# Optimization experiments

Measured on AMD Instinct MI355X. Metric: run time of the kernel, lower is better.

The kernel has to match this reference:

```python
import jax, jax.numpy as jnp
import numpy as np

B, S, D = 1, 2048, 4096
NH, NKV, HD = 32, 8, 128
N_REP = NH // NKV
NEG = -1e9


def setup_inputs() -> dict:
    key = jax.random.key(0)
    ks = jax.random.split(key, 8)
    x = jax.random.normal(ks[0], (B, S, D), dtype=jnp.float32)
    # rotary freqs (theta=10000), shape [S, HD//2]
    inv = 1.0 / (10000.0 ** (jnp.arange(0, HD, 2, dtype=jnp.float32) / HD))
    ang = jnp.arange(S, dtype=jnp.float32)[:, None] * inv[None, :]
    freqs_cos, freqs_sin = jnp.cos(ang), jnp.sin(ang)
    # causal mask [1,1,S,S]
    row = jnp.arange(S)[:, None]
    col = jnp.arange(S)[None, :]
    mask = jnp.where(col <= row, 0.0, NEG).astype(jnp.float32)[None, None]
    input_indexes = jnp.arange(S, dtype=jnp.int64)
    cache_k = jnp.zeros((B, S, NKV, HD), dtype=jnp.float32)
    cache_v = jnp.zeros((B, S, NKV, HD), dtype=jnp.float32)
    sc = 0.02
    wq = jax.random.normal(ks[1], (NH * HD, D), dtype=jnp.float32) * sc
    wk = jax.random.normal(ks[2], (NKV * HD, D), dtype=jnp.float32) * sc
    wv = jax.random.normal(ks[3], (NKV * HD, D), dtype=jnp.float32) * sc
    wo = jax.random.normal(ks[4], (NH * HD, D), dtype=jnp.float32).T * sc
    return {"x": x, "freqs_cos": freqs_cos, "freqs_sin": freqs_sin, "mask": mask,
            "input_indexes": input_indexes, "cache_k": cache_k, "cache_v": cache_v,
            "wq": wq, "wk": wk, "wv": wv, "wo": wo}


def _rope(t, cos, sin):
    # t: [B,S,H,HD]; treat last dim as HD//2 complex pairs (even=real, odd=imag)
    tr = t.reshape(*t.shape[:-1], HD // 2, 2)
    xr, xi = tr[..., 0], tr[..., 1]
    c = cos[None, :, None, :]  # [1,S,1,HD//2]
    s = sin[None, :, None, :]
    outr = xr * c - xi * s
    outi = xr * s + xi * c
    return jnp.stack([outr, outi], axis=-1).reshape(t.shape)


def reference(x, freqs_cos, freqs_sin, mask, input_indexes, cache_k, cache_v, wq, wk, wv, wo):
    bsz, seqlen = x.shape[0], x.shape[-2]
    xq = (x @ wq.T).reshape(bsz, seqlen, NH, HD)
    xk = (x @ wk.T).reshape(bsz, seqlen, NKV, HD)
    xv = (x @ wv.T).reshape(bsz, seqlen, NKV, HD)
    xq = _rope(xq, freqs_cos, freqs_sin)
    xk = _rope(xk, freqs_cos, freqs_sin)
    # KV-cache append (index_copy along seq dim)
    cache_k = cache_k.at[:, input_indexes].set(xk)
    cache_v = cache_v.at[:, input_indexes].set(xv)
    # GQA: repeat kv heads
    keys = jnp.repeat(cache_k, N_REP, axis=2)    # [B,S,NH,HD]
    values = jnp.repeat(cache_v, N_REP, axis=2)
    scores = jnp.einsum('bshd,bthd->bhst', xq, keys) / jnp.sqrt(jnp.float32(HD))
    scores = scores + mask
    probs = jax.nn.softmax(scores.astype(jnp.float32), axis=-1).astype(xq.dtype)
    out = jnp.einsum('bhst,bthd->bhsd', probs, values)
    out = out.transpose(0, 2, 1, 3).reshape(bsz, seqlen, -1)
    return (out @ wo.T, cache_k, cache_v)
```

## Files before the change

### kernel.cpp

```cpp
#include <hip/hip_runtime.h>
#include <cstdint>

#define S_LEN 2048
#define D_DIM 4096
#define NH_ 32
#define NKV_ 8
#define HD_ 128
#define GK 4096

typedef unsigned short u16;
typedef __attribute__((ext_vector_type(4))) float f32x4;
typedef __attribute__((ext_vector_type(8))) short bf16x8;
typedef __attribute__((ext_vector_type(4))) short s16x4;

__device__ __forceinline__ short f2bf(float f) {
  union { float f; unsigned int u; } v; v.f = f;
  unsigned int r = v.u + 0x7fffu + ((v.u >> 16) & 1u);
  return (short)(r >> 16);
}

__device__ __forceinline__ void glds16(const void* g, void* l) {
  __builtin_amdgcn_global_load_lds(
      (const __attribute__((address_space(1))) void*)g,
      (__attribute__((address_space(3))) void*)l, 16, 0, 0);
}

__global__ __launch_bounds__(256) void cvt_bf16(const float* __restrict__ src,
                                                u16* __restrict__ dst, int n8) {
  int i = blockIdx.x * 256 + threadIdx.x;
  if (i < n8) {
    float4 a = *(const float4*)&src[(size_t)i * 8];
    float4 b = *(const float4*)&src[(size_t)i * 8 + 4];
    bf16x8 o = { f2bf(a.x), f2bf(a.y), f2bf(a.z), f2bf(a.w),
                 f2bf(b.x), f2bf(b.y), f2bf(b.z), f2bf(b.w) };
    *(bf16x8*)&dst[(size_t)i * 8] = o;
  }
}

template <int MODE>
__global__ __launch_bounds__(256) void gemm_bf(const u16* __restrict__ A,
                                               const u16* __restrict__ W,
                                               float* __restrict__ C,
                                               u16* __restrict__ qbf,
                                               u16* __restrict__ kbf,
                                               u16* __restrict__ vbf,
                                               float* __restrict__ cko,
                                               float* __restrict__ cvo,
                                               const float* __restrict__ fc,
                                               const float* __restrict__ fs,
                                               int N) {
  __shared__ __align__(16) u16 As[128 * 64];
  __shared__ __align__(16) u16 Bs[128 * 64];
  const int t = threadIdx.x;
  const int lane = t & 63;
  const int wave = t >> 6;
  const int wm = (wave >> 1) * 64;
  const int wn = (wave & 1) * 64;
  const int quad = lane >> 4;
  const int L = lane & 15;
  const int bm = blockIdx.y * 128;
  const int bn = blockIdx.x * 128;
  const int dr = lane >> 3;
  const int cb = lane & 7;
  const int cbs = cb ^ dr;

  f32x4 acc[4][4];
#pragma unroll
  for (int i = 0; i < 4; ++i)
#pragma unroll
    for (int j = 0; j < 4; ++j) { f32x4 z = {0.f, 0.f, 0.f, 0.f}; acc[i][j] = z; }

  for (int k0 = 0; k0 < GK; k0 += 64) {
    __syncthreads();
#pragma unroll
    for (int q = 0; q < 4; ++q) {
      int chunk = wave * 4 + q;
      int row = chunk * 8 + dr;
      glds16(&A[(size_t)(bm + row) * GK + k0 + cbs * 8], &As[chunk * 512]);
      glds16(&W[(size_t)(bn + row) * GK + k0 + cbs * 8], &Bs[chunk * 512]);
    }
    __syncthreads();
#pragma unroll
    for (int s = 0; s < 2; ++s) {
      bf16x8 af[4], bw[4];
#pragma unroll
      for (int i = 0; i < 4; ++i)
        af[i] = *(const bf16x8*)&As[(wm + 16 * i + L) * 64 + (((s * 4 + quad) ^ (L & 7)) * 8)];
#pragma unroll
      for (int j = 0; j < 4; ++j)
        bw[j] = *(const bf16x8*)&Bs[(wn + 16 * j + L) * 64 + (((s * 4 + quad) ^ (L & 7)) * 8)];
#pragma unroll
      for (int i = 0; i < 4; ++i)
#pragma unroll
        for (int j = 0; j < 4; ++j)
          acc[i][j] = __builtin_amdgcn_mfma_f32_16x16x32_bf16(af[i], bw[j], acc[i][j], 0, 0, 0);
    }
  }

  if (MODE == 0) {
#pragma unroll
    for (int i = 0; i < 4; ++i) {
      int r0 = bm + wm + i * 16 + quad * 4;
#pragma unroll
      for (int j = 0; j < 4; ++j) {
        int c = bn + wn + j * 16 + L;
#pragma unroll
        for (int r = 0; r < 4; ++r) C[(size_t)(r0 + r) * N + c] = acc[i][j][r];
      }
    }
  } else {
    const float scale = 0.08838834764831845f;
#pragma unroll
    for (int i = 0; i < 4; ++i) {
#pragma unroll
      for (int j = 0; j < 4; ++j) {
        int c = bn + wn + 16 * j + L;
#pragma unroll
        for (int r = 0; r < 4; ++r) {
          int srow = bm + wm + 16 * i + 4 * quad + r;
          float v = acc[i][j][r];
          float partner = __shfl_xor(v, 1);
          if (c < 4096) {
            int p = (c >> 1) & 63;
            float co = fc[srow * 64 + p], si = fs[srow * 64 + p];
            float out = (c & 1) ? partner * si + v * co : v * co - partner * si;
            qbf[(size_t)srow * 4096 + c] = (u16)f2bf(out * scale);
          } else if (c < 5120) {
            int p = (c >> 1) & 63;
            float co = fc[srow * 64 + p], si = fs[srow * 64 + p];
            float out = (c & 1) ? partner * si + v * co : v * co - partner * si;
            int cc = c - 4096;
            cko[(size_t)srow * 1024 + cc] = out;
            kbf[(size_t)srow * 1024 + cc] = (u16)f2bf(out);
          } else {
            int cc = c - 5120;
            cvo[(size_t)srow * 1024 + cc] = v;
            vbf[(size_t)srow * 1024 + cc] = (u16)f2bf(v);
          }
        }
      }
    }
  }
}

__global__ __launch_bounds__(256, 3) void attn_bf(const u16* __restrict__ qbf,
                                                  const u16* __restrict__ kbf,
                                                  const u16* __restrict__ vbf,
                                                  u16* __restrict__ ao) {
  __shared__ __align__(16) u16 Ks[64 * 136];
  __shared__ __align__(16) u16 Vt[128 * 64];
  __shared__ __align__(16) u16 Ps[4 * 16 * 72];
  const int t = threadIdx.x;
  const int wave = t >> 6;
  const int lane = t & 63;
  const int Q4 = lane >> 4;
  const int L = lane & 15;
  const int h = blockIdx.y;
  const int qb = 31 - (int)blockIdx.x;
  const int kvh = h >> 2;
  const int qs0 = qb * 64;
  u16* Psw = &Ps[wave * 16 * 72];

  bf16x8 qf[4];
  {
    const u16* qbase = &qbf[(size_t)(qs0 + 16 * wave + L) * D_DIM + h * HD_ + 8 * Q4];
#pragma unroll
    for (int s = 0; s < 4; ++s) qf[s] = *(const bf16x8*)&qbase[32 * s];
  }

  f32x4 o[8];
#pragma unroll
  for (int jd = 0; jd < 8; ++jd) { f32x4 z = {0.f, 0.f, 0.f, 0.f}; o[jd] = z; }
  float mold[4] = {-1e30f, -1e30f, -1e30f, -1e30f};
  float lst[4] = {0.f, 0.f, 0.f, 0.f};

  for (int kt = 0; kt <= qb; ++kt) {
    __syncthreads();
    const u16* kb = &kbf[(size_t)(kt * 64) * (NKV_ * HD_) + kvh * HD_];
    const u16* vb = &vbf[(size_t)(kt * 64) * (NKV_ * HD_) + kvh * HD_];
#pragma unroll
    for (int p = 0; p < 4; ++p) {
      int u = t + 256 * p;
      int r = u >> 4, c8 = u & 15;
      *(bf16x8*)&Ks[r * 136 + c8 * 8] =
          *(const bf16x8*)&kb[(size_t)r * (NKV_ * HD_) + c8 * 8];
    }
#pragma unroll
    for (int p = 0; p < 4; ++p) {
      int u = t + 256 * p;
      int d = u & 127, bb = u >> 7;
      const u16* vsrc = &vb[(size_t)(bb * 8) * (NKV_ * HD_) + d];
      short vv[8];
#pragma unroll
      for (int j = 0; j < 8; ++j) vv[j] = (short)vsrc[(size_t)j * (NKV_ * HD_)];
      bf16x8 pk = { vv[0], vv[1], vv[2], vv[3], vv[4], vv[5], vv[6], vv[7] };
      *(bf16x8*)&Vt[d * 64 + ((bb + d) & 7) * 8] = pk;
    }
    __syncthreads();

    f32x4 sa[4];
#pragma unroll
    for (int jn = 0; jn < 4; ++jn) { f32x4 z = {0.f, 0.f, 0.f, 0.f}; sa[jn] = z; }
#pragma unroll
    for (int s = 0; s < 4; ++s) {
#pragma unroll
      for (int jn = 0; jn < 4; ++jn) {
        bf16x8 kf = *(const bf16x8*)&Ks[(16 * jn + L) * 136 + 32 * s + 8 * Q4];
        sa[jn] = __builtin_amdgcn_mfma_f32_16x16x32_bf16(qf[s], kf, sa[jn], 0, 0, 0);
      }
    }

    const int gq0 = qs0 + 16 * wave + 4 * Q4;
    const int gk0 = kt * 64 + L;
    float rmax[4];
#pragma unroll
    for (int r = 0; r < 4; ++r) {
#pragma unroll
      for (int jn = 0; jn < 4; ++jn)
        if (gk0 + 16 * jn > gq0 + r) sa[jn][r] = -1e30f;
      rmax[r] = fmaxf(fmaxf(sa[0][r], sa[1][r]), fmaxf(sa[2][r], sa[3][r]));
    }
#pragma unroll
    for (int m = 1; m < 16; m <<= 1) {
#pragma unroll
      for (int r = 0; r < 4; ++r) rmax[r] = fmaxf(rmax[r], __shfl_xor(rmax[r], m));
    }
    float p_[4][4], rsum[4], alpha[4];
#pragma unroll
    for (int r = 0; r < 4; ++r) {
      float mnew = fmaxf(mold[r], rmax[r]);
      alpha[r] = __expf(mold[r] - mnew);
#pragma unroll
      for (int jn = 0; jn < 4; ++jn) p_[jn][r] = __expf(sa[jn][r] - mnew);
      rsum[r] = (p_[0][r] + p_[1][r]) + (p_[2][r] + p_[3][r]);
      mold[r] = mnew;
    }
#pragma unroll
    for (int m = 1; m < 16; m <<= 1) {
#pragma unroll
      for (int r = 0; r < 4; ++r) rsum[r] += __shfl_xor(rsum[r], m);
    }
#pragma unroll
    for (int r = 0; r < 4; ++r) lst[r] = lst[r] * alpha[r] + rsum[r];
#pragma unroll
    for (int jd = 0; jd < 8; ++jd)
#pragma unroll
      for (int r = 0; r < 4; ++r) o[jd][r] *= alpha[r];

#pragma unroll
    for (int r = 0; r < 4; ++r)
#pragma unroll
      for (int jn = 0; jn < 4; ++jn)
        Psw[(4 * Q4 + r) * 72 + 16 * jn + L] = (u16)f2bf(p_[jn][r]);
    asm volatile("s_waitcnt lgkmcnt(0)" ::: "memory");

#pragma unroll
    for (int s2 = 0; s2 < 2; ++s2) {
      bf16x8 pa = *(const bf16x8*)&Psw[L * 72 + 32 * s2 + 8 * Q4];
#pragma unroll
      for (int jd = 0; jd < 8; ++jd) {
        bf16x8 vf = *(const bf16x8*)&Vt[(16 * jd + L) * 64 + ((4 * s2 + Q4 + L) & 7) * 8];
        o[jd] = __builtin_amdgcn_mfma_f32_16x16x32_bf16(pa, vf, o[jd], 0, 0, 0);
      }
    }
  }

  float inv[4];
#pragma unroll
  for (int r = 0; r < 4; ++r) inv[r] = 1.0f / lst[r];
#pragma unroll
  for (int r = 0; r < 4; ++r) {
    u16* dst = &ao[(size_t)(qs0 + 16 * wave + 4 * Q4 + r) * D_DIM + h * HD_ + L];
#pragma unroll
    for (int jd = 0; jd < 8; ++jd) dst[16 * jd] = (u16)f2bf(o[jd][r] * inv[r]);
  }
}

#define LDA 40
__global__ __launch_bounds__(256) void gemm_bt(const float* __restrict__ A,
                                               const float* __restrict__ W,
                                               float* __restrict__ C, int N) {
  __shared__ short As[128 * LDA];
  __shared__ short Bs[128 * LDA];
  const int t = threadIdx.x;
  const int lane = t & 63;
  const int wave = t >> 6;
  const int wm = (wave >> 1) * 64;
  const int wn = (wave & 1) * 64;
  const int quad = lane >> 4;
  const int l15 = lane & 15;
  const int bm = blockIdx.y * 128;
  const int bn = blockIdx.x * 128;
  f32x4 acc[4][4];
#pragma unroll
  for (int i = 0; i < 4; ++i)
#pragma unroll
    for (int j = 0; j < 4; ++j) { f32x4 z = {0.f, 0.f, 0.f, 0.f}; acc[i][j] = z; }
  for (int k0 = 0; k0 < GK; k0 += 32) {
    __syncthreads();
#pragma unroll
    for (int p = 0; p < 4; ++p) {
      int idx = p * 256 + t;
      int row = idx >> 3;
      int c4 = (idx & 7) * 4;
      const float4 av = *(const float4*)&A[(size_t)(bm + row) * GK + k0 + c4];
      const float4 wv = *(const float4*)&W[(size_t)(bn + row) * GK + k0 + c4];
      s16x4 a4 = { f2bf(av.x), f2bf(av.y), f2bf(av.z), f2bf(av.w) };
      s16x4 w4 = { f2bf(wv.x), f2bf(wv.y), f2bf(wv.z), f2bf(wv.w) };
      *(s16x4*)&As[row * LDA + c4] = a4;
      *(s16x4*)&Bs[row * LDA + c4] = w4;
    }
    __syncthreads();
    bf16x8 af[4], bfr[4];
#pragma unroll
    for (int i = 0; i < 4; ++i) {
      af[i]  = *(const bf16x8*)&As[(wm + i * 16 + l15) * LDA + quad * 8];
      bfr[i] = *(const bf16x8*)&Bs[(wn + i * 16 + l15) * LDA + quad * 8];
    }
#pragma unroll
    for (int i = 0; i < 4; ++i)
#pragma unroll
      for (int j = 0; j < 4; ++j)
        acc[i][j] = __builtin_amdgcn_mfma_f32_16x16x32_bf16(af[i], bfr[j], acc[i][j], 0, 0, 0);
  }
#pragma unroll
  for (int i = 0; i < 4; ++i) {
    int r0 = bm + wm + i * 16 + quad * 4;
#pragma unroll
    for (int j = 0; j < 4; ++j) {
      int c = bn + wn + j * 16 + l15;
#pragma unroll
      for (int r = 0; r < 4; ++r) C[(size_t)(r0 + r) * N + c] = acc[i][j][r];
    }
  }
}

__global__ __launch_bounds__(256) void rope_kernel(float* __restrict__ xq,
                                                   const float* __restrict__ xk,
                                                   float* __restrict__ cko,
                                                   const float* __restrict__ fc,
                                                   const float* __restrict__ fs) {
  int i = blockIdx.x * 256 + threadIdx.x;
  const int NQP = S_LEN * NH_ * (HD_ / 2);
  if (i < NQP) {
    int s = i >> 11; int rem = i & 2047; int p = rem & 63;
    float c = fc[s * 64 + p], sn = fs[s * 64 + p];
    float2 v = *(const float2*)&xq[(size_t)s * D_DIM + 2 * rem];
    *(float2*)&xq[(size_t)s * D_DIM + 2 * rem] =
        make_float2(v.x * c - v.y * sn, v.x * sn + v.y * c);
  } else {
    int j = i - NQP; int s = j >> 9; int rem = j & 511; int p = rem & 63;
    float c = fc[s * 64 + p], sn = fs[s * 64 + p];
    float2 v = *(const float2*)&xk[(size_t)s * (NKV_ * HD_) + 2 * rem];
    *(float2*)&cko[(size_t)s * (NKV_ * HD_) + 2 * rem] =
        make_float2(v.x * c - v.y * sn, v.x * sn + v.y * c);
  }
}

__global__ __launch_bounds__(256, 3) void attn_mfma(const float* __restrict__ xq,
                                                    const float* __restrict__ ck,
                                                    const float* __restrict__ cv,
                                                    float* __restrict__ outp) {
  __shared__ __align__(16) short Ks[64 * 136];
  __shared__ __align__(16) short Vt[128 * 64];
  __shared__ __align__(16) short Ps[4 * 16 * 72];
  const int t = threadIdx.x;
  const int wave = t >> 6;
  const int lane = t & 63;
  const int Q4 = lane >> 4;
  const int L = lane & 15;
  const int h = blockIdx.y;
  const int qb = 31 - (int)blockIdx.x;
  const int kvh = h >> 2;
  const int qs0 = qb * 64;
  const float scale = 0.08838834764831845f;
  short* Psw = &Ps[wave * 16 * 72];
  bf16x8 qf[4];
  {
    const float* qbase = &xq[(size_t)(qs0 + 16 * wave + L) * D_DIM + h * HD_ + 8 * Q4];
#pragma unroll
    for (int s = 0; s < 4; ++s) {
      float4 a = *(const float4*)&qbase[32 * s];
      float4 b = *(const float4*)&qbase[32 * s + 4];
      bf16x8 q8 = { f2bf(a.x * scale), f2bf(a.y * scale), f2bf(a.z * scale), f2bf(a.w * scale),
                    f2bf(b.x * scale), f2bf(b.y * scale), f2bf(b.z * scale), f2bf(b.w * scale) };
      qf[s] = q8;
    }
  }
  f32x4 o[8];
#pragma unroll
  for (int jd = 0; jd < 8; ++jd) { f32x4 z = {0.f, 0.f, 0.f, 0.f}; o[jd] = z; }
  float mold[4] = {-1e30f, -1e30f, -1e30f, -1e30f};
  float lst[4] = {0.f, 0.f, 0.f, 0.f};
  for (int kt = 0; kt <= qb; ++kt) {
    __syncthreads();
    const float* ckb = &ck[(size_t)(kt * 64) * (NKV_ * HD_) + kvh * HD_];
    const float* cvb = &cv[(size_t)(kt * 64) * (NKV_ * HD_) + kvh * HD_];
#pragma unroll
    for (int p = 0; p < 8; ++p) {
      int i = t + 256 * p;
      int r = i >> 5, c4 = (i & 31) * 4;
      float4 v = *(const float4*)&ckb[(size_t)r * (NKV_ * HD_) + c4];
      s16x4 k4 = { f2bf(v.x), f2bf(v.y), f2bf(v.z), f2bf(v.w) };
      *(s16x4*)&Ks[r * 136 + c4] = k4;
    }
#pragma unroll
    for (int p = 0; p < 4; ++p) {
      int u = t + 256 * p;
      int d = u & 127, bb = u >> 7;
      float vv[8];
#pragma unroll
      for (int j = 0; j < 8; ++j) vv[j] = cvb[(size_t)(bb * 8 + j) * (NKV_ * HD_) + d];
      bf16x8 pk = { f2bf(vv[0]), f2bf(vv[1]), f2bf(vv[2]), f2bf(vv[3]),
                    f2bf(vv[4]), f2bf(vv[5]), f2bf(vv[6]), f2bf(vv[7]) };
      *(bf16x8*)&Vt[d * 64 + ((bb + d) & 7) * 8] = pk;
    }
    __syncthreads();
    f32x4 sa[4];
#pragma unroll
    for (int jn = 0; jn < 4; ++jn) { f32x4 z = {0.f, 0.f, 0.f, 0.f}; sa[jn] = z; }
#pragma unroll
    for (int s = 0; s < 4; ++s) {
#pragma unroll
      for (int jn = 0; jn < 4; ++jn) {
        bf16x8 kf = *(const bf16x8*)&Ks[(16 * jn + L) * 136 + 32 * s + 8 * Q4];
        sa[jn] = __builtin_amdgcn_mfma_f32_16x16x32_bf16(qf[s], kf, sa[jn], 0, 0, 0);
      }
    }
    const int gq0 = qs0 + 16 * wave + 4 * Q4;
    const int gk0 = kt * 64 + L;
    float rmax[4];
#pragma unroll
    for (int r = 0; r < 4; ++r) {
#pragma unroll
      for (int jn = 0; jn < 4; ++jn)
        if (gk0 + 16 * jn > gq0 + r) sa[jn][r] = -1e30f;
      rmax[r] = fmaxf(fmaxf(sa[0][r], sa[1][r]), fmaxf(sa[2][r], sa[3][r]));
    }
#pragma unroll
    for (int m = 1; m < 16; m <<= 1) {
#pragma unroll
      for (int r = 0; r < 4; ++r) rmax[r] = fmaxf(rmax[r], __shfl_xor(rmax[r], m));
    }
    float p_[4][4], rsum[4], alpha[4];
#pragma unroll
    for (int r = 0; r < 4; ++r) {
      float mnew = fmaxf(mold[r], rmax[r]);
      alpha[r] = __expf(mold[r] - mnew);
#pragma unroll
      for (int jn = 0; jn < 4; ++jn) p_[jn][r] = __expf(sa[jn][r] - mnew);
      rsum[r] = (p_[0][r] + p_[1][r]) + (p_[2][r] + p_[3][r]);
      mold[r] = mnew;
    }
#pragma unroll
    for (int m = 1; m < 16; m <<= 1) {
#pragma unroll
      for (int r = 0; r < 4; ++r) rsum[r] += __shfl_xor(rsum[r], m);
    }
#pragma unroll
    for (int r = 0; r < 4; ++r) lst[r] = lst[r] * alpha[r] + rsum[r];
#pragma unroll
    for (int jd = 0; jd < 8; ++jd)
#pragma unroll
      for (int r = 0; r < 4; ++r) o[jd][r] *= alpha[r];
#pragma unroll
    for (int r = 0; r < 4; ++r)
#pragma unroll
      for (int jn = 0; jn < 4; ++jn)
        Psw[(4 * Q4 + r) * 72 + 16 * jn + L] = f2bf(p_[jn][r]);
    asm volatile("s_waitcnt lgkmcnt(0)" ::: "memory");
#pragma unroll
    for (int s2 = 0; s2 < 2; ++s2) {
      bf16x8 pa = *(const bf16x8*)&Psw[L * 72 + 32 * s2 + 8 * Q4];
#pragma unroll
      for (int jd = 0; jd < 8; ++jd) {
        bf16x8 vf = *(const bf16x8*)&Vt[(16 * jd + L) * 64 + ((4 * s2 + Q4 + L) & 7) * 8];
        o[jd] = __builtin_amdgcn_mfma_f32_16x16x32_bf16(pa, vf, o[jd], 0, 0, 0);
      }
    }
  }
  float inv[4];
#pragma unroll
  for (int r = 0; r < 4; ++r) inv[r] = 1.0f / lst[r];
#pragma unroll
  for (int r = 0; r < 4; ++r) {
    float* dst = &outp[(size_t)(qs0 + 16 * wave + 4 * Q4 + r) * D_DIM + h * HD_ + L];
#pragma unroll
    for (int jd = 0; jd < 8; ++jd) dst[16 * jd] = o[jd][r] * inv[r];
  }
}

extern "C" void kernel_launch(void* const* d_in, const int* in_sizes, int n_in,
                              void* d_out, int out_size, void* d_ws, size_t ws_size,
                              hipStream_t stream) {
  (void)in_sizes; (void)n_in; (void)out_size;
  const float* x  = (const float*)d_in[0];
  const float* fc = (const float*)d_in[1];
  const float* fs = (const float*)d_in[2];
  const float* wq = (const float*)d_in[7];
  const float* wk = (const float*)d_in[8];
  const float* wv = (const float*)d_in[9];
  const float* wo = (const float*)d_in[10];
  float* outp = (float*)d_out;
  float* ck = outp + (size_t)S_LEN * D_DIM;
  float* cv = ck + (size_t)S_LEN * NKV_ * HD_;

  if (ws_size >= 109051904ull) {
    u16* x_bf = (u16*)d_ws;
    u16* wqkv = x_bf + 8388608;
    u16* q_bf = wqkv + 25165824;
    u16* k_bf = q_bf + 8388608;
    u16* v_bf = k_bf + 2097152;
    u16* ao_bf = v_bf + 2097152;
    u16* wo_bf = wqkv;

    cvt_bf16<<<4096, 256, 0, stream>>>(x, x_bf, 1048576);
    cvt_bf16<<<8192, 256, 0, stream>>>(wq, wqkv, 2097152);
    cvt_bf16<<<2048, 256, 0, stream>>>(wk, wqkv + 16777216, 524288);
    cvt_bf16<<<2048, 256, 0, stream>>>(wv, wqkv + 20971520, 524288);
    gemm_bf<1><<<dim3(48, 16), 256, 0, stream>>>(x_bf, wqkv, nullptr, q_bf,
                                                 k_bf, v_bf, ck, cv, fc, fs, 6144);
    cvt_bf16<<<8192, 256, 0, stream>>>(wo, wo_bf, 2097152);
    attn_bf<<<dim3(32, 32), 256, 0, stream>>>(q_bf, k_bf, v_bf, ao_bf);
    gemm_bf<0><<<dim3(32, 16), 256, 0, stream>>>(ao_bf, wo_bf, outp, nullptr,
                                                 nullptr, nullptr, nullptr,
                                                 nullptr, fc, fs, 4096);
  } else {
    float* xq = (float*)d_ws;
    float* xk = xq + (size_t)S_LEN * D_DIM;
    dim3 blk(256);
    gemm_bt<<<dim3(32, 16), blk, 0, stream>>>(x, wq, xq, 4096);
    gemm_bt<<<dim3(8, 16),  blk, 0, stream>>>(x, wk, xk, 1024);
    gemm_bt<<<dim3(8, 16),  blk, 0, stream>>>(x, wv, cv, 1024);
    rope_kernel<<<20480, 256, 0, stream>>>(xq, xk, ck, fc, fs);
    attn_mfma<<<dim3(32, 32), 512 / 2, 0, stream>>>(xq, ck, cv, xq);
    gemm_bt<<<dim3(32, 16), blk, 0, stream>>>(xq, wo, outp, 4096);
  }
}
```

Measured before the change: 650.3 us.

## Split-K GEMMs with reduce kernels, fuse conversions and overlap Wo cast

Both projection GEMMs now split the K dimension into two halves over a z grid dimension and write fp32 partials. Separate reduce kernels sum the halves and apply RoPE, scaling, bf16 conversion and the KV-cache writes. This doubles the number of blocks so more of the device's CUs are occupied. The four input conversions are merged into one launch, and the Wo conversion runs in an extra grid row of the QKV GEMM. In exchange it adds large fp32 partial-buffer traffic, two extra reduce passes and a much larger workspace requirement; the old fp32 fallback path is removed.

New measurement: 702.4 us. 8.0% more time.

```diff
diff --git a/kernel.cpp b/kernel.cpp
--- a/kernel.cpp
+++ b/kernel.cpp
@@ -23,6 +23,301 @@
   __builtin_amdgcn_global_load_lds(
       (const __attribute__((address_space(1))) void*)g,
       (__attribute__((address_space(3))) void*)l, 16, 0, 0);
+}
+
+__global__ __launch_bounds__(256) void cvt_all(const float* __restrict__ x,
+                                               const float* __restrict__ wq,
+                                               const float* __restrict__ wk,
+                                               const float* __restrict__ wv,
+                                               u16* __restrict__ xbf,
+                                               u16* __restrict__ wqkv) {
+  size_t u = (size_t)blockIdx.x * 256 + threadIdx.x;
+  const float* src;
+  u16* dst;
+  if (u < 1048576u) { src = x + u * 8; dst = xbf + u * 8; }
+  else if (u < 3145728u) { size_t o = u - 1048576u; src = wq + o * 8; dst = wqkv + o * 8; }
+  else if (u < 3670016u) { size_t o = u - 3145728u; src = wk + o * 8; dst = wqkv + 16777216u + o * 8; }
+  else { size_t o = u - 3670016u; src = wv + o * 8; dst = wqkv + 20971520u + o * 8; }
+  float4 a = *(const float4*)src;
+  float4 b = *(const float4*)(src + 4);
+  bf16x8 o8 = { f2bf(a.x), f2bf(a.y), f2bf(a.z), f2bf(a.w),
+                f2bf(b.x), f2bf(b.y), f2bf(b.z), f2bf(b.w) };
+  *(bf16x8*)dst = o8;
+}
+
+template <int FUSED>
+__global__ __launch_bounds__(256) void gemm_ps(const u16* __restrict__ A,
+                                               const u16* __restrict__ W,
+                                               float* __restrict__ P, int N,
+                                               const float* __restrict__ wo_src,
+                                               u16* __restrict__ wo_dst) {
+  __shared__ __align__(16) u16 As[128 * 64];
+  __shared__ __align__(16) u16 Bs[128 * 64];
+  if (FUSED && blockIdx.y == 16) {
+    size_t r = blockIdx.x + 48u * blockIdx.z;
+    for (size_t u = r * 256 + threadIdx.x; u < 2097152u; u += 96u * 256u) {
+      float4 a = *(const float4*)&wo_src[u * 8];
+      float4 b = *(const float4*)&wo_src[u * 8 + 4];
+      bf16x8 o8 = { f2bf(a.x), f2bf(a.y), f2bf(a.z), f2bf(a.w),
+                    f2bf(b.x), f2bf(b.y), f2bf(b.z), f2bf(b.w) };
+      *(bf16x8*)&wo_dst[u * 8] = o8;
+    }
+    return;
+  }
+  const int t = threadIdx.x;
+  const int lane = t & 63;
+  const int wave = t >> 6;
+  const int wm = (wave >> 1) * 64;
+  const int wn = (wave & 1) * 64;
+  const int quad = lane >> 4;
+  const int L = lane & 15;
+  const int bm = blockIdx.y * 128;
+  const int bn = blockIdx.x * 128;
+  const int z = blockIdx.z;
+  const int dr = lane >> 3;
+  const int cb = lane & 7;
+  const int cbs = cb ^ dr;
+
+  f32x4 acc[4][4];
+#pragma unroll
+  for (int i = 0; i < 4; ++i)
+#pragma unroll
+    for (int j = 0; j < 4; ++j) { f32x4 zz = {0.f, 0.f, 0.f, 0.f}; acc[i][j] = zz; }
+
+  const int kbeg = z * 2048, kend = kbeg + 2048;
+  for (int k0 = kbeg; k0 < kend; k0 += 64) {
+    __syncthreads();
+#pragma unroll
+    for (int q = 0; q < 4; ++q) {
+      int chunk = wave * 4 + q;
+      int row = chunk * 8 + dr;
+      glds16(&A[(size_t)(bm + row) * GK + k0 + cbs * 8], &As[chunk * 512]);
+      glds16(&W[(size_t)(bn + row) * GK + k0 + cbs * 8], &Bs[chunk * 512]);
+    }
+    __syncthreads();
+#pragma unroll
+    for (int s = 0; s < 2; ++s) {
+      bf16x8 af[4], bw[4];
+#pragma unroll
+      for (int i = 0; i < 4; ++i)
+        af[i] = *(const bf16x8*)&As[(wm + 16 * i + L) * 64 + (((s * 4 + quad) ^ (L & 7)) * 8)];
+#pragma unroll
+      for (int j = 0; j < 4; ++j)
+        bw[j] = *(const bf16x8*)&Bs[(wn + 16 * j + L) * 64 + (((s * 4 + quad) ^ (L & 7)) * 8)];
+#pragma unroll
+      for (int i = 0; i < 4; ++i)
+#pragma unroll
+        for (int j = 0; j < 4; ++j)
+          acc[i][j] = __builtin_amdgcn_mfma_f32_16x16x32_bf16(af[i], bw[j], acc[i][j], 0, 0, 0);
+    }
+  }
+  float* Pz = P + (size_t)z * 2048 * N;
+#pragma unroll
+  for (int i = 0; i < 4; ++i) {
+    int r0 = bm + wm + i * 16 + quad * 4;
+#pragma unroll
+    for (int j = 0; j < 4; ++j) {
+      int c = bn + wn + j * 16 + L;
+#pragma unroll
+      for (int r = 0; r < 4; ++r) Pz[(size_t)(r0 + r) * N + c] = acc[i][j][r];
+    }
+  }
+}
+
+__global__ __launch_bounds__(256) void reduce_qkv(const float* __restrict__ P,
+                                                  u16* __restrict__ qbf,
+                                                  u16* __restrict__ kbf,
+                                                  u16* __restrict__ vbf,
+                                                  float* __restrict__ cko,
+                                                  float* __restrict__ cvo,
+                                                  const float* __restrict__ fc,
+                                                  const float* __restrict__ fs) {
+  int u = blockIdx.x * 256 + threadIdx.x;
+  int row = u / 768;
+  int c0 = (u - row * 768) * 8;
+  const float* p0 = &P[(size_t)row * 6144 + c0];
+  const float* p1 = p0 + 12582912u;
+  float4 a0 = *(const float4*)p0, b0 = *(const float4*)(p0 + 4);
+  float4 a1 = *(const float4*)p1, b1 = *(const float4*)(p1 + 4);
+  float v[8] = { a0.x + a1.x, a0.y + a1.y, a0.z + a1.z, a0.w + a1.w,
+                 b0.x + b1.x, b0.y + b1.y, b0.z + b1.z, b0.w + b1.w };
+  const float scale = 0.08838834764831845f;
+  if (c0 < 5120) {
+    float o[8];
+#pragma unroll
+    for (int j = 0; j < 8; j += 2) {
+      int p = ((c0 + j) >> 1) & 63;
+      float co = fc[row * 64 + p], si = fs[row * 64 + p];
+      o[j]     = v[j] * co - v[j + 1] * si;
+      o[j + 1] = v[j] * si + v[j + 1] * co;
+    }
+    if (c0 < 4096) {
+      bf16x8 q8 = { f2bf(o[0] * scale), f2bf(o[1] * scale), f2bf(o[2] * scale), f2bf(o[3] * scale),
+                    f2bf(o[4] * scale), f2bf(o[5] * scale), f2bf(o[6] * scale), f2bf(o[7] * scale) };
+      *(bf16x8*)&qbf[(size_t)row * 4096 + c0] = q8;
+    } else {
+      int cc = c0 - 4096;
+      bf16x8 k8 = { f2bf(o[0]), f2bf(o[1]), f2bf(o[2]), f2bf(o[3]),
+                    f2bf(o[4]), f2bf(o[5]), f2bf(o[6]), f2bf(o[7]) };
+      *(bf16x8*)&kbf[(size_t)row * 1024 + cc] = k8;
+      float* cd = &cko[(size_t)row * 1024 + cc];
+      *(float4*)cd = make_float4(o[0], o[1], o[2], o[3]);
+      *(float4*)(cd + 4) = make_float4(o[4], o[5], o[6], o[7]);
+    }
+  } else {
+    int cc = c0 - 5120;
+    bf16x8 v8 = { f2bf(v[0]), f2bf(v[1]), f2bf(v[2]), f2bf(v[3]),
+                  f2bf(v[4]), f2bf(v[5]), f2bf(v[6]), f2bf(v[7]) };
+    *(bf16x8*)&vbf[(size_t)row * 1024 + cc] = v8;
+    float* cd = &cvo[(size_t)row * 1024 + cc];
+    *(float4*)cd = make_float4(v[0], v[1], v[2], v[3]);
+    *(float4*)(cd + 4) = make_float4(v[4], v[5], v[6], v[7]);
+  }
+}
+
+__global__ __launch_bounds__(256) void reduce_o(const float* __restrict__ P,
+                                                float* __restrict__ out) {
+  size_t u = (size_t)blockIdx.x * 256 + threadIdx.x;
+  const float* p0 = &P[u * 8];
+  const float* p1 = p0 + 8388608u;
+  float4 a0 = *(const float4*)p0, b0 = *(const float4*)(p0 + 4);
+  float4 a1 = *(const float4*)p1, b1 = *(const float4*)(p1 + 4);
+  float* d = &out[u * 8];
+  *(float4*)d = make_float4(a0.x + a1.x, a0.y + a1.y, a0.z + a1.z, a0.w + a1.w);
+  *(float4*)(d + 4) = make_float4(b0.x + b1.x, b0.y + b1.y, b0.z + b1.z, b0.w + b1.w);
+}
+
+__global__ __launch_bounds__(256, 3) void attn_bf(const u16* __restrict__ qbf,
+                                                  const u16* __restrict__ kbf,
+                                                  const u16* __restrict__ vbf,
+                                                  u16* __restrict__ ao) {
+  __shared__ __align__(16) u16 Ks[64 * 136];
+  __shared__ __align__(16) u16 Vt[128 * 64];
+  __shared__ __align__(16) u16 Ps[4 * 16 * 72];
+  const int t = threadIdx.x;
+  const int wave = t >> 6;
+  const int lane = t & 63;
+  const int Q4 = lane >> 4;
+  const int L = lane & 15;
+  const int h = blockIdx.y;
+  const int qb = 31 - (int)blockIdx.x;
+  const int kvh = h >> 2;
+  const int qs0 = qb * 64;
+  u16* Psw = &Ps[wave * 16 * 72];
+
+  bf16x8 qf[4];
+  {
+    const u16* qbase = &qbf[(size_t)(qs0 + 16 * wave + L) * D_DIM + h * HD_ + 8 * Q4];
+#pragma unroll
+    for (int s = 0; s < 4; ++s) qf[s] = *(const bf16x8*)&qbase[32 * s];
+  }
+
+  f32x4 o[8];
+#pragma unroll
+  for (int jd = 0; jd < 8; ++jd) { f32x4 z = {0.f, 0.f, 0.f, 0.f}; o[jd] = z; }
+  float mold[4] = {-1e30f, -1e30f, -1e30f, -1e30f};
+  float lst[4] = {0.f, 0.f, 0.f, 0.f};
+
+  for (int kt = 0; kt <= qb; ++kt) {
+    __syncthreads();
+    const u16* kb = &kbf[(size_t)(kt * 64) * (NKV_ * HD_) + kvh * HD_];
+    const u16* vb = &vbf[(size_t)(kt * 64) * (NKV_ * HD_) + kvh * HD_];
+#pragma unroll
+    for (int p = 0; p < 4; ++p) {
+      int u = t + 256 * p;
+      int r = u >> 4, c8 = u & 15;
+      *(bf16x8*)&Ks[r * 136 + c8 * 8] =
+          *(const bf16x8*)&kb[(size_t)r * (NKV_ * HD_) + c8 * 8];
+    }
+#pragma unroll
+    for (int p = 0; p < 4; ++p) {
+      int u = t + 256 * p;
+      int d = u & 127, bb = u >> 7;
+      const u16* vsrc = &vb[(size_t)(bb * 8) * (NKV_ * HD_) + d];
+      short vv[8];
+#pragma unroll
+      for (int j = 0; j < 8; ++j) vv[j] = (short)vsrc[(size_t)j * (NKV_ * HD_)];
+      bf16x8 pk = { vv[0], vv[1], vv[2], vv[3], vv[4], vv[5], vv[6], vv[7] };
+      *(bf16x8*)&Vt[d * 64 + ((bb + d) & 7) * 8] = pk;
+    }
+    __syncthreads();
+
+    f32x4 sa[4];
+#pragma unroll
+    for (int jn = 0; jn < 4; ++jn) { f32x4 z = {0.f, 0.f, 0.f, 0.f}; sa[jn] = z; }
+#pragma unroll
+    for (int s = 0; s < 4; ++s) {
+#pragma unroll
+      for (int jn = 0; jn < 4; ++jn) {
+        bf16x8 kf = *(const bf16x8*)&Ks[(16 * jn + L) * 136 + 32 * s + 8 * Q4];
+        sa[jn] = __builtin_amdgcn_mfma_f32_16x16x32_bf16(qf[s], kf, sa[jn], 0, 0, 0);
+      }
+    }
+
+    const int gq0 = qs0 + 16 * wave + 4 * Q4;
+    const int gk0 = kt * 64 + L;
+    float rmax[4];
+#pragma unroll
+    for (int r = 0; r < 4; ++r) {
+#pragma unroll
+      for (int jn = 0; jn < 4; ++jn)
+        if (gk0 + 16 * jn > gq0 + r) sa[jn][r] = -1e30f;
+      rmax[r] = fmaxf(fmaxf(sa[0][r], sa[1][r]), fmaxf(sa[2][r], sa[3][r]));
+    }
+#pragma unroll
+    for (int m = 1; m < 16; m <<= 1) {
+#pragma unroll
+      for (int r = 0; r < 4; ++r) rmax[r] = fmaxf(rmax[r], __shfl_xor(rmax[r], m));
+    }
+    float p_[4][4], rsum[4], alpha[4];
+#pragma unroll
+    for (int r = 0; r < 4; ++r) {
+      float mnew = fmaxf(mold[r], rmax[r]);
+      alpha[r] = __expf(mold[r] - mnew);
+#pragma unroll
+      for (int jn = 0; jn < 4; ++jn) p_[jn][r] = __expf(sa[jn][r] - mnew);
+      rsum[r] = (p_[0][r] + p_[1][r]) + (p_[2][r] + p_[3][r]);
+      mold[r] = mnew;
+    }
+#pragma unroll
+    for (int m = 1; m < 16; m <<= 1) {
+#pragma unroll
+      for (int r = 0; r < 4; ++r) rsum[r] += __shfl_xor(rsum[r], m);
+    }
+#pragma unroll
+    for (int r = 0; r < 4; ++r) lst[r] = lst[r] * alpha[r] + rsum[r];
+#pragma unroll
+    for (int jd = 0; jd < 8; ++jd)
+#pragma unroll
+      for (int r = 0; r < 4; ++r) o[jd][r] *= alpha[r];
+
+#pragma unroll
+    for (int r = 0; r < 4; ++r)
+#pragma unroll
+      for (int jn = 0; jn < 4; ++jn)
+        Psw[(4 * Q4 + r) * 72 + 16 * jn + L] = (u16)f2bf(p_[jn][r]);
+    asm volatile("s_waitcnt lgkmcnt(0)" ::: "memory");
+
+#pragma unroll
+    for (int s2 = 0; s2 < 2; ++s2) {
+      bf16x8 pa = *(const bf16x8*)&Psw[L * 72 + 32 * s2 + 8 * Q4];
+#pragma unroll
+      for (int jd = 0; jd < 8; ++jd) {
+        bf16x8 vf = *(const bf16x8*)&Vt[(16 * jd + L) * 64 + ((4 * s2 + Q4 + L) & 7) * 8];
+        o[jd] = __builtin_amdgcn_mfma_f32_16x16x32_bf16(pa, vf, o[jd], 0, 0, 0);
+      }
+    }
+  }
+
+  float inv[4];
+#pragma unroll
+  for (int r = 0; r < 4; ++r) inv[r] = 1.0f / lst[r];
+#pragma unroll
+  for (int r = 0; r < 4; ++r) {
+    u16* dst = &ao[(size_t)(qs0 + 16 * wave + 4 * Q4 + r) * D_DIM + h * HD_ + L];
+#pragma unroll
+    for (int jd = 0; jd < 8; ++jd) dst[16 * jd] = (u16)f2bf(o[jd][r] * inv[r]);
+  }
 }
 
 __global__ __launch_bounds__(256) void cvt_bf16(const float* __restrict__ src,
@@ -63,13 +358,11 @@
   const int dr = lane >> 3;
   const int cb = lane & 7;
   const int cbs = cb ^ dr;
-
   f32x4 acc[4][4];
 #pragma unroll
   for (int i = 0; i < 4; ++i)
 #pragma unroll
     for (int j = 0; j < 4; ++j) { f32x4 z = {0.f, 0.f, 0.f, 0.f}; acc[i][j] = z; }
-
   for (int k0 = 0; k0 < GK; k0 += 64) {
     __syncthreads();
 #pragma unroll
@@ -96,7 +389,6 @@
           acc[i][j] = __builtin_amdgcn_mfma_f32_16x16x32_bf16(af[i], bw[j], acc[i][j], 0, 0, 0);
     }
   }
-
   if (MODE == 0) {
 #pragma unroll
     for (int i = 0; i < 4; ++i) {
@@ -143,353 +435,6 @@
   }
 }
 
-__global__ __launch_bounds__(256, 3) void attn_bf(const u16* __restrict__ qbf,
-                                                  const u16* __restrict__ kbf,
-                                                  const u16* __restrict__ vbf,
-                                                  u16* __restrict__ ao) {
-  __shared__ __align__(16) u16 Ks[64 * 136];
-  __shared__ __align__(16) u16 Vt[128 * 64];
-  __shared__ __align__(16) u16 Ps[4 * 16 * 72];
-  const int t = threadIdx.x;
-  const int wave = t >> 6;
-  const int lane = t & 63;
-  const int Q4 = lane >> 4;
-  const int L = lane & 15;
-  const int h = blockIdx.y;
-  const int qb = 31 - (int)blockIdx.x;
-  const int kvh = h >> 2;
-  const int qs0 = qb * 64;
-  u16* Psw = &Ps[wave * 16 * 72];
-
-  bf16x8 qf[4];
-  {
-    const u16* qbase = &qbf[(size_t)(qs0 + 16 * wave + L) * D_DIM + h * HD_ + 8 * Q4];
-#pragma unroll
-    for (int s = 0; s < 4; ++s) qf[s] = *(const bf16x8*)&qbase[32 * s];
-  }
-
-  f32x4 o[8];
-#pragma unroll
-  for (int jd = 0; jd < 8; ++jd) { f32x4 z = {0.f, 0.f, 0.f, 0.f}; o[jd] = z; }
-  float mold[4] = {-1e30f, -1e30f, -1e30f, -1e30f};
-  float lst[4] = {0.f, 0.f, 0.f, 0.f};
-
-  for (int kt = 0; kt <= qb; ++kt) {
-    __syncthreads();
-    const u16* kb = &kbf[(size_t)(kt * 64) * (NKV_ * HD_) + kvh * HD_];
-    const u16* vb = &vbf[(size_t)(kt * 64) * (NKV_ * HD_) + kvh * HD_];
-#pragma unroll
-    for (int p = 0; p < 4; ++p) {
-      int u = t + 256 * p;
-      int r = u >> 4, c8 = u & 15;
-      *(bf16x8*)&Ks[r * 136 + c8 * 8] =
-          *(const bf16x8*)&kb[(size_t)r * (NKV_ * HD_) + c8 * 8];
-    }
-#pragma unroll
-    for (int p = 0; p < 4; ++p) {
-      int u = t + 256 * p;
-      int d = u & 127, bb = u >> 7;
-      const u16* vsrc = &vb[(size_t)(bb * 8) * (NKV_ * HD_) + d];
-      short vv[8];
-#pragma unroll
-      for (int j = 0; j < 8; ++j) vv[j] = (short)vsrc[(size_t)j * (NKV_ * HD_)];
-      bf16x8 pk = { vv[0], vv[1], vv[2], vv[3], vv[4], vv[5], vv[6], vv[7] };
-      *(bf16x8*)&Vt[d * 64 + ((bb + d) & 7) * 8] = pk;
-    }
-    __syncthreads();
-
-    f32x4 sa[4];
-#pragma unroll
-    for (int jn = 0; jn < 4; ++jn) { f32x4 z = {0.f, 0.f, 0.f, 0.f}; sa[jn] = z; }
-#pragma unroll
-    for (int s = 0; s < 4; ++s) {
-#pragma unroll
-      for (int jn = 0; jn < 4; ++jn) {
-        bf16x8 kf = *(const bf16x8*)&Ks[(16 * jn + L) * 136 + 32 * s + 8 * Q4];
-        sa[jn] = __builtin_amdgcn_mfma_f32_16x16x32_bf16(qf[s], kf, sa[jn], 0, 0, 0);
-      }
-    }
-
-    const int gq0 = qs0 + 16 * wave + 4 * Q4;
-    const int gk0 = kt * 64 + L;
-    float rmax[4];
-#pragma unroll
-    for (int r = 0; r < 4; ++r) {
-#pragma unroll
-      for (int jn = 0; jn < 4; ++jn)
-        if (gk0 + 16 * jn > gq0 + r) sa[jn][r] = -1e30f;
-      rmax[r] = fmaxf(fmaxf(sa[0][r], sa[1][r]), fmaxf(sa[2][r], sa[3][r]));
-    }
-#pragma unroll
-    for (int m = 1; m < 16; m <<= 1) {
-#pragma unroll
-      for (int r = 0; r < 4; ++r) rmax[r] = fmaxf(rmax[r], __shfl_xor(rmax[r], m));
-    }
-    float p_[4][4], rsum[4], alpha[4];
-#pragma unroll
-    for (int r = 0; r < 4; ++r) {
-      float mnew = fmaxf(mold[r], rmax[r]);
-      alpha[r] = __expf(mold[r] - mnew);
-#pragma unroll
-      for (int jn = 0; jn < 4; ++jn) p_[jn][r] = __expf(sa[jn][r] - mnew);
-      rsum[r] = (p_[0][r] + p_[1][r]) + (p_[2][r] + p_[3][r]);
-      mold[r] = mnew;
-    }
-#pragma unroll
-    for (int m = 1; m < 16; m <<= 1) {
-#pragma unroll
-      for (int r = 0; r < 4; ++r) rsum[r] += __shfl_xor(rsum[r], m);
-    }
-#pragma unroll
-    for (int r = 0; r < 4; ++r) lst[r] = lst[r] * alpha[r] + rsum[r];
-#pragma unroll
-    for (int jd = 0; jd < 8; ++jd)
-#pragma unroll
-      for (int r = 0; r < 4; ++r) o[jd][r] *= alpha[r];
-
-#pragma unroll
-    for (int r = 0; r < 4; ++r)
-#pragma unroll
-      for (int jn = 0; jn < 4; ++jn)
-        Psw[(4 * Q4 + r) * 72 + 16 * jn + L] = (u16)f2bf(p_[jn][r]);
-    asm volatile("s_waitcnt lgkmcnt(0)" ::: "memory");
-
-#pragma unroll
-    for (int s2 = 0; s2 < 2; ++s2) {
-      bf16x8 pa = *(const bf16x8*)&Psw[L * 72 + 32 * s2 + 8 * Q4];
-#pragma unroll
-      for (int jd = 0; jd < 8; ++jd) {
-        bf16x8 vf = *(const bf16x8*)&Vt[(16 * jd + L) * 64 + ((4 * s2 + Q4 + L) & 7) * 8];
-        o[jd] = __builtin_amdgcn_mfma_f32_16x16x32_bf16(pa, vf, o[jd], 0, 0, 0);
-      }
-    }
-  }
-
-  float inv[4];
-#pragma unroll
-  for (int r = 0; r < 4; ++r) inv[r] = 1.0f / lst[r];
-#pragma unroll
-  for (int r = 0; r < 4; ++r) {
-    u16* dst = &ao[(size_t)(qs0 + 16 * wave + 4 * Q4 + r) * D_DIM + h * HD_ + L];
-#pragma unroll
-    for (int jd = 0; jd < 8; ++jd) dst[16 * jd] = (u16)f2bf(o[jd][r] * inv[r]);
-  }
-}
-
-#define LDA 40
-__global__ __launch_bounds__(256) void gemm_bt(const float* __restrict__ A,
-                                               const float* __restrict__ W,
-                                               float* __restrict__ C, int N) {
-  __shared__ short As[128 * LDA];
-  __shared__ short Bs[128 * LDA];
-  const int t = threadIdx.x;
-  const int lane = t & 63;
-  const int wave = t >> 6;
-  const int wm = (wave >> 1) * 64;
-  const int wn = (wave & 1) * 64;
-  const int quad = lane >> 4;
-  const int l15 = lane & 15;
-  const int bm = blockIdx.y * 128;
-  const int bn = blockIdx.x * 128;
-  f32x4 acc[4][4];
-#pragma unroll
-  for (int i = 0; i < 4; ++i)
-#pragma unroll
-    for (int j = 0; j < 4; ++j) { f32x4 z = {0.f, 0.f, 0.f, 0.f}; acc[i][j] = z; }
-  for (int k0 = 0; k0 < GK; k0 += 32) {
-    __syncthreads();
-#pragma unroll
-    for (int p = 0; p < 4; ++p) {
-      int idx = p * 256 + t;
-      int row = idx >> 3;
-      int c4 = (idx & 7) * 4;
-      const float4 av = *(const float4*)&A[(size_t)(bm + row) * GK + k0 + c4];
-      const float4 wv = *(const float4*)&W[(size_t)(bn + row) * GK + k0 + c4];
-      s16x4 a4 = { f2bf(av.x), f2bf(av.y), f2bf(av.z), f2bf(av.w) };
-      s16x4 w4 = { f2bf(wv.x), f2bf(wv.y), f2bf(wv.z), f2bf(wv.w) };
-      *(s16x4*)&As[row * LDA + c4] = a4;
-      *(s16x4*)&Bs[row * LDA + c4] = w4;
-    }
-    __syncthreads();
-    bf16x8 af[4], bfr[4];
-#pragma unroll
-    for (int i = 0; i < 4; ++i) {
-      af[i]  = *(const bf16x8*)&As[(wm + i * 16 + l15) * LDA + quad * 8];
-      bfr[i] = *(const bf16x8*)&Bs[(wn + i * 16 + l15) * LDA + quad * 8];
-    }
-#pragma unroll
-    for (int i = 0; i < 4; ++i)
-#pragma unroll
-      for (int j = 0; j < 4; ++j)
-        acc[i][j] = __builtin_amdgcn_mfma_f32_16x16x32_bf16(af[i], bfr[j], acc[i][j], 0, 0, 0);
-  }
-#pragma unroll
-  for (int i = 0; i < 4; ++i) {
-    int r0 = bm + wm + i * 16 + quad * 4;
-#pragma unroll
-    for (int j = 0; j < 4; ++j) {
-      int c = bn + wn + j * 16 + l15;
-#pragma unroll
-      for (int r = 0; r < 4; ++r) C[(size_t)(r0 + r) * N + c] = acc[i][j][r];
-    }
-  }
-}
-
-__global__ __launch_bounds__(256) void rope_kernel(float* __restrict__ xq,
-                                                   const float* __restrict__ xk,
-                                                   float* __restrict__ cko,
-                                                   const float* __restrict__ fc,
-                                                   const float* __restrict__ fs) {
-  int i = blockIdx.x * 256 + threadIdx.x;
-  const int NQP = S_LEN * NH_ * (HD_ / 2);
-  if (i < NQP) {
-    int s = i >> 11; int rem = i & 2047; int p = rem & 63;
-    float c = fc[s * 64 + p], sn = fs[s * 64 + p];
-    float2 v = *(const float2*)&xq[(size_t)s * D_DIM + 2 * rem];
-    *(float2*)&xq[(size_t)s * D_DIM + 2 * rem] =
-        make_float2(v.x * c - v.y * sn, v.x * sn + v.y * c);
-  } else {
-    int j = i - NQP; int s = j >> 9; int rem = j & 511; int p = rem & 63;
-    float c = fc[s * 64 + p], sn = fs[s * 64 + p];
-    float2 v = *(const float2*)&xk[(size_t)s * (NKV_ * HD_) + 2 * rem];
-    *(float2*)&cko[(size_t)s * (NKV_ * HD_) + 2 * rem] =
-        make_float2(v.x * c - v.y * sn, v.x * sn + v.y * c);
-  }
-}
-
-__global__ __launch_bounds__(256, 3) void attn_mfma(const float* __restrict__ xq,
-                                                    const float* __restrict__ ck,
-                                                    const float* __restrict__ cv,
-                                                    float* __restrict__ outp) {
-  __shared__ __align__(16) short Ks[64 * 136];
-  __shared__ __align__(16) short Vt[128 * 64];
-  __shared__ __align__(16) short Ps[4 * 16 * 72];
-  const int t = threadIdx.x;
-  const int wave = t >> 6;
-  const int lane = t & 63;
-  const int Q4 = lane >> 4;
-  const int L = lane & 15;
-  const int h = blockIdx.y;
-  const int qb = 31 - (int)blockIdx.x;
-  const int kvh = h >> 2;
-  const int qs0 = qb * 64;
-  const float scale = 0.08838834764831845f;
-  short* Psw = &Ps[wave * 16 * 72];
-  bf16x8 qf[4];
-  {
-    const float* qbase = &xq[(size_t)(qs0 + 16 * wave + L) * D_DIM + h * HD_ + 8 * Q4];
-#pragma unroll
-    for (int s = 0; s < 4; ++s) {
-      float4 a = *(const float4*)&qbase[32 * s];
-      float4 b = *(const float4*)&qbase[32 * s + 4];
-      bf16x8 q8 = { f2bf(a.x * scale), f2bf(a.y * scale), f2bf(a.z * scale), f2bf(a.w * scale),
-                    f2bf(b.x * scale), f2bf(b.y * scale), f2bf(b.z * scale), f2bf(b.w * scale) };
-      qf[s] = q8;
-    }
-  }
-  f32x4 o[8];
-#pragma unroll
-  for (int jd = 0; jd < 8; ++jd) { f32x4 z = {0.f, 0.f, 0.f, 0.f}; o[jd] = z; }
-  float mold[4] = {-1e30f, -1e30f, -1e30f, -1e30f};
-  float lst[4] = {0.f, 0.f, 0.f, 0.f};
-  for (int kt = 0; kt <= qb; ++kt) {
-    __syncthreads();
-    const float* ckb = &ck[(size_t)(kt * 64) * (NKV_ * HD_) + kvh * HD_];
-    const float* cvb = &cv[(size_t)(kt * 64) * (NKV_ * HD_) + kvh * HD_];
-#pragma unroll
-    for (int p = 0; p < 8; ++p) {
-      int i = t + 256 * p;
-      int r = i >> 5, c4 = (i & 31) * 4;
-      float4 v = *(const float4*)&ckb[(size_t)r * (NKV_ * HD_) + c4];
-      s16x4 k4 = { f2bf(v.x), f2bf(v.y), f2bf(v.z), f2bf(v.w) };
-      *(s16x4*)&Ks[r * 136 + c4] = k4;
-    }
-#pragma unroll
-    for (int p = 0; p < 4; ++p) {
-      int u = t + 256 * p;
-      int d = u & 127, bb = u >> 7;
-      float vv[8];
-#pragma unroll
-      for (int j = 0; j < 8; ++j) vv[j] = cvb[(size_t)(bb * 8 + j) * (NKV_ * HD_) + d];
-      bf16x8 pk = { f2bf(vv[0]), f2bf(vv[1]), f2bf(vv[2]), f2bf(vv[3]),
-                    f2bf(vv[4]), f2bf(vv[5]), f2bf(vv[6]), f2bf(vv[7]) };
-      *(bf16x8*)&Vt[d * 64 + ((bb + d) & 7) * 8] = pk;
-    }
-    __syncthreads();
-    f32x4 sa[4];
-#pragma unroll
-    for (int jn = 0; jn < 4; ++jn) { f32x4 z = {0.f, 0.f, 0.f, 0.f}; sa[jn] = z; }
-#pragma unroll
-    for (int s = 0; s < 4; ++s) {
-#pragma unroll
-      for (int jn = 0; jn < 4; ++jn) {
-        bf16x8 kf = *(const bf16x8*)&Ks[(16 * jn + L) * 136 + 32 * s + 8 * Q4];
-        sa[jn] = __builtin_amdgcn_mfma_f32_16x16x32_bf16(qf[s], kf, sa[jn], 0, 0, 0);
-      }
-    }
-    const int gq0 = qs0 + 16 * wave + 4 * Q4;
-    const int gk0 = kt * 64 + L;
-    float rmax[4];
-#pragma unroll
-    for (int r = 0; r < 4; ++r) {
-#pragma unroll
-      for (int jn = 0; jn < 4; ++jn)
-        if (gk0 + 16 * jn > gq0 + r) sa[jn][r] = -1e30f;
-      rmax[r] = fmaxf(fmaxf(sa[0][r], sa[1][r]), fmaxf(sa[2][r], sa[3][r]));
-    }
-#pragma unroll
-    for (int m = 1; m < 16; m <<= 1) {
-#pragma unroll
-      for (int r = 0; r < 4; ++r) rmax[r] = fmaxf(rmax[r], __shfl_xor(rmax[r], m));
-    }
-    float p_[4][4], rsum[4], alpha[4];
-#pragma unroll
-    for (int r = 0; r < 4; ++r) {
-      float mnew = fmaxf(mold[r], rmax[r]);
-      alpha[r] = __expf(mold[r] - mnew);
-#pragma unroll
-      for (int jn = 0; jn < 4; ++jn) p_[jn][r] = __expf(sa[jn][r] - mnew);
-      rsum[r] = (p_[0][r] + p_[1][r]) + (p_[2][r] + p_[3][r]);
-      mold[r] = mnew;
-    }
-#pragma unroll
-    for (int m = 1; m < 16; m <<= 1) {
-#pragma unroll
-      for (int r = 0; r < 4; ++r) rsum[r] += __shfl_xor(rsum[r], m);
-    }
-#pragma unroll
-    for (int r = 0; r < 4; ++r) lst[r] = lst[r] * alpha[r] + rsum[r];
-#pragma unroll
-    for (int jd = 0; jd < 8; ++jd)
-#pragma unroll
-      for (int r = 0; r < 4; ++r) o[jd][r] *= alpha[r];
-#pragma unroll
-    for (int r = 0; r < 4; ++r)
-#pragma unroll
-      for (int jn = 0; jn < 4; ++jn)
-        Psw[(4 * Q4 + r) * 72 + 16 * jn + L] = f2bf(p_[jn][r]);
-    asm volatile("s_waitcnt lgkmcnt(0)" ::: "memory");
-#pragma unroll
-    for (int s2 = 0; s2 < 2; ++s2) {
-      bf16x8 pa = *(const bf16x8*)&Psw[L * 72 + 32 * s2 + 8 * Q4];
-#pragma unroll
-      for (int jd = 0; jd < 8; ++jd) {
-        bf16x8 vf = *(const bf16x8*)&Vt[(16 * jd + L) * 64 + ((4 * s2 + Q4 + L) & 7) * 8];
-        o[jd] = __builtin_amdgcn_mfma_f32_16x16x32_bf16(pa, vf, o[jd], 0, 0, 0);
-      }
-    }
-  }
-  float inv[4];
-#pragma unroll
-  for (int r = 0; r < 4; ++r) inv[r] = 1.0f / lst[r];
-#pragma unroll
-  for (int r = 0; r < 4; ++r) {
-    float* dst = &outp[(size_t)(qs0 + 16 * wave + 4 * Q4 + r) * D_DIM + h * HD_ + L];
-#pragma unroll
-    for (int jd = 0; jd < 8; ++jd) dst[16 * jd] = o[jd][r] * inv[r];
-  }
-}
-
 extern "C" void kernel_launch(void* const* d_in, const int* in_sizes, int n_in,
                               void* d_out, int out_size, void* d_ws, size_t ws_size,
                               hipStream_t stream) {
@@ -505,19 +450,35 @@
   float* ck = outp + (size_t)S_LEN * D_DIM;
   float* cv = ck + (size_t)S_LEN * NKV_ * HD_;
 
-  if (ws_size >= 109051904ull) {
+  if (ws_size >= 243269632ull) {
+    u16* x_bf  = (u16*)d_ws;
+    u16* wqkv  = x_bf + 8388608u;
+    u16* wo_bf = wqkv + 25165824u;
+    u16* q_bf  = wo_bf + 16777216u;
+    u16* k_bf  = q_bf + 8388608u;
+    u16* v_bf  = k_bf + 2097152u;
+    u16* ao_bf = v_bf + 2097152u;
+    float* part = (float*)(ao_bf + 8388608u);
+
+    cvt_all<<<16384, 256, 0, stream>>>(x, wq, wk, wv, x_bf, wqkv);
+    gemm_ps<1><<<dim3(48, 17, 2), 256, 0, stream>>>(x_bf, wqkv, part, 6144, wo, wo_bf);
+    reduce_qkv<<<6144, 256, 0, stream>>>(part, q_bf, k_bf, v_bf, ck, cv, fc, fs);
+    attn_bf<<<dim3(32, 32), 256, 0, stream>>>(q_bf, k_bf, v_bf, ao_bf);
+    gemm_ps<0><<<dim3(32, 16, 2), 256, 0, stream>>>(ao_bf, wo_bf, part, 4096, nullptr, nullptr);
+    reduce_o<<<4096, 256, 0, stream>>>(part, outp);
+  } else {
     u16* x_bf = (u16*)d_ws;
-    u16* wqkv = x_bf + 8388608;
-    u16* q_bf = wqkv + 25165824;
-    u16* k_bf = q_bf + 8388608;
-    u16* v_bf = k_bf + 2097152;
-    u16* ao_bf = v_bf + 2097152;
+    u16* wqkv = x_bf + 8388608u;
+    u16* q_bf = wqkv + 25165824u;
+    u16* k_bf = q_bf + 8388608u;
+    u16* v_bf = k_bf + 2097152u;
+    u16* ao_bf = v_bf + 2097152u;
     u16* wo_bf = wqkv;
 
     cvt_bf16<<<4096, 256, 0, stream>>>(x, x_bf, 1048576);
     cvt_bf16<<<8192, 256, 0, stream>>>(wq, wqkv, 2097152);
-    cvt_bf16<<<2048, 256, 0, stream>>>(wk, wqkv + 16777216, 524288);
-    cvt_bf16<<<2048, 256, 0, stream>>>(wv, wqkv + 20971520, 524288);
+    cvt_bf16<<<2048, 256, 0, stream>>>(wk, wqkv + 16777216u, 524288);
+    cvt_bf16<<<2048, 256, 0, stream>>>(wv, wqkv + 20971520u, 524288);
     gemm_bf<1><<<dim3(48, 16), 256, 0, stream>>>(x_bf, wqkv, nullptr, q_bf,
                                                  k_bf, v_bf, ck, cv, fc, fs, 6144);
     cvt_bf16<<<8192, 256, 0, stream>>>(wo, wo_bf, 2097152);
@@ -525,15 +486,5 @@
     gemm_bf<0><<<dim3(32, 16), 256, 0, stream>>>(ao_bf, wo_bf, outp, nullptr,
                                                  nullptr, nullptr, nullptr,
                                                  nullptr, fc, fs, 4096);
-  } else {
-    float* xq = (float*)d_ws;
-    float* xk = xq + (size_t)S_LEN * D_DIM;
-    dim3 blk(256);
-    gemm_bt<<<dim3(32, 16), blk, 0, stream>>>(x, wq, xq, 4096);
-    gemm_bt<<<dim3(8, 16),  blk, 0, stream>>>(x, wk, xk, 1024);
-    gemm_bt<<<dim3(8, 16),  blk, 0, stream>>>(x, wv, cv, 1024);
-    rope_kernel<<<20480, 256, 0, stream>>>(xq, xk, ck, fc, fs);
-    attn_mfma<<<dim3(32, 32), 512 / 2, 0, stream>>>(xq, ck, cv, xq);
-    gemm_bt<<<dim3(32, 16), blk, 0, stream>>>(xq, wo, outp, 4096);
-  }
-}
+  }
+}
```
